# Performance work log

Hardware: AMD Instinct MI355X
Metric: run time of the kernel (lower is better)

Reference implementation:

```python
import jax, jax.numpy as jnp
import numpy as np

D_MODEL = 1024
D_FF = 4096
NUM_EXPERTS = 8
TOP_K = 2


def setup_inputs() -> dict:
    key = jax.random.key(0)
    ks = jax.random.split(key, 9)
    s_in = 1.0 / np.sqrt(D_MODEL)
    s_ff = 1.0 / np.sqrt(D_FF)
    return {
        "x": jax.random.normal(ks[0], (2, 1024, D_MODEL), dtype=jnp.float32),
        "Wg": jax.random.uniform(ks[1], (D_MODEL, NUM_EXPERTS), minval=-s_in, maxval=s_in, dtype=jnp.float32),
        "bg": jax.random.uniform(ks[2], (NUM_EXPERTS,), minval=-s_in, maxval=s_in, dtype=jnp.float32),
        "W1": jax.random.uniform(ks[3], (NUM_EXPERTS, D_MODEL, D_FF), minval=-s_in, maxval=s_in, dtype=jnp.float32),
        "b1": jax.random.uniform(ks[4], (NUM_EXPERTS, D_FF), minval=-s_in, maxval=s_in, dtype=jnp.float32),
        "W2": jax.random.uniform(ks[5], (NUM_EXPERTS, D_MODEL, D_FF), minval=-s_in, maxval=s_in, dtype=jnp.float32),
        "b2": jax.random.uniform(ks[6], (NUM_EXPERTS, D_FF), minval=-s_in, maxval=s_in, dtype=jnp.float32),
        "W3": jax.random.uniform(ks[7], (NUM_EXPERTS, D_FF, D_MODEL), minval=-s_ff, maxval=s_ff, dtype=jnp.float32),
        "b3": jax.random.uniform(ks[8], (NUM_EXPERTS, D_MODEL), minval=-s_ff, maxval=s_ff, dtype=jnp.float32),
    }


def reference(x, Wg, bg, W1, b1, W2, b2, W3, b3):
    B, S, D = x.shape
    xf = x.reshape(-1, D)                                   # [N, D]
    N = xf.shape[0]

    # ---- Router (eval mode: no noise) ----
    logits = xf @ Wg + bg                                   # [N, E]
    top_logits, top_idx = jax.lax.top_k(logits, TOP_K)      # [N, K]
    top_w = jax.nn.softmax(top_logits, axis=-1)             # softmax over the top-k logits
    # scatter top-k weights into dense [N, E]; indices are unique per row
    comb_w = jnp.zeros_like(logits).at[jnp.arange(N)[:, None], top_idx].set(top_w)

    # ---- Experts: GLU-MLP, dense per-expert (weights are 0 for unrouted tokens) ----
    h1 = jnp.einsum('nd,edf->enf', xf, W1) + b1[:, None, :]  # [E, N, F]
    h2 = jnp.einsum('nd,edf->enf', xf, W2) + b2[:, None, :]
    hidden = jax.nn.gelu(h1, approximate=False) * h2         # torch nn.GELU is exact (erf)
    expert_out = jnp.einsum('enf,efd->end', hidden, W3) + b3[:, None, :]  # [E, N, D]

    # ---- Weighted combine ----
    final = jnp.einsum('end,ne->nd', expert_out, comb_w)     # [N, D]
    aux_loss = 0.0  # eval mode: aux loss inactive
    return final.reshape(B, S, D), aux_loss
```

## Files before the change

### kernel.cpp

```cpp
#include <hip/hip_runtime.h>
#include <hip/hip_bf16.h>
#include <math.h>

#define D_MODEL 1024
#define D_FF    4096
#define NE      8
#define MT      256

typedef __bf16 bf16x8 __attribute__((ext_vector_type(8)));
typedef float  f32x4  __attribute__((ext_vector_type(4)));

__device__ __forceinline__ void async16(const void* g, void* l) {
    __builtin_amdgcn_global_load_lds(
        (__attribute__((address_space(1))) uint32_t*)g,
        (__attribute__((address_space(3))) uint32_t*)l, 16, 0, 0);
}

__device__ __forceinline__ void transpose_tile64(
    const float* __restrict__ s, __bf16* __restrict__ d,
    int K, int N, int kt, int nt, int tid, float (*tile)[65])
{
    int tr = tid >> 4, tc = (tid & 15) * 4;
#pragma unroll
    for (int it = 0; it < 4; ++it) {
        float4 v = *reinterpret_cast<const float4*>(
            s + (size_t)(kt + tr + it * 16) * N + nt + tc);
        tile[tr + it * 16][tc + 0] = v.x;
        tile[tr + it * 16][tc + 1] = v.y;
        tile[tr + it * 16][tc + 2] = v.z;
        tile[tr + it * 16][tc + 3] = v.w;
    }
    __syncthreads();
    int kq = (tid & 15) * 4;
#pragma unroll
    for (int it = 0; it < 4; ++it) {
        int rr = (tid >> 4) + it * 16;
        union { __bf16 h[4]; ushort4 u; } pk;
        pk.h[0] = (__bf16)tile[kq + 0][rr];
        pk.h[1] = (__bf16)tile[kq + 1][rr];
        pk.h[2] = (__bf16)tile[kq + 2][rr];
        pk.h[3] = (__bf16)tile[kq + 3][rr];
        *reinterpret_cast<ushort4*>(d + (size_t)(nt + rr) * K + kt + kq) = pk.u;
    }
}

__global__ __launch_bounds__(256) void fused_pre(
    const float* __restrict__ x, const float* __restrict__ Wg,
    const float* __restrict__ bg, int* __restrict__ topidx,
    float* __restrict__ topw, __bf16* __restrict__ Xb,
    const float* __restrict__ W1, const float* __restrict__ W2,
    const float* __restrict__ W3,
    __bf16* __restrict__ W1t, __bf16* __restrict__ W2t,
    __bf16* __restrict__ W3t, int nrouter)
{
    __shared__ float buf[64][65];
    int bid = blockIdx.x, tid = threadIdx.x;

    if (bid >= nrouter) {
        int tt = bid - nrouter;
        if (tt < 2 * 8192) {
            const float* s = W1; __bf16* d = W1t;
            if (tt >= 8192) { s = W2; d = W2t; tt -= 8192; }
            int e = tt >> 10, rem = tt & 1023;
            int kt_i = rem >> 6, nt_i = rem & 63;
            transpose_tile64(s + ((size_t)e << 22), d + ((size_t)e << 22),
                             D_MODEL, D_FF, kt_i * 64, nt_i * 64, tid, buf);
        } else {
            tt -= 2 * 8192;
            int e = tt >> 10, rem = tt & 1023;
            int kt_i = rem >> 4, nt_i = rem & 15;
            transpose_tile64(W3 + ((size_t)e << 22), W3t + ((size_t)e << 22),
                             D_FF, D_MODEL, kt_i * 64, nt_i * 64, tid, buf);
        }
        return;
    }

    int n = bid;
    const float* xr = x + (size_t)n * D_MODEL;
    int d0 = tid * 4;
    float4 xv = *reinterpret_cast<const float4*>(xr + d0);

    union { __bf16 h[4]; ushort4 u; } pk;
    pk.h[0] = (__bf16)xv.x; pk.h[1] = (__bf16)xv.y;
    pk.h[2] = (__bf16)xv.z; pk.h[3] = (__bf16)xv.w;
    *reinterpret_cast<ushort4*>(Xb + (size_t)n * D_MODEL + d0) = pk.u;

    float part[NE];
#pragma unroll
    for (int e = 0; e < NE; ++e) part[e] = 0.f;
    float xs[4] = {xv.x, xv.y, xv.z, xv.w};
#pragma unroll
    for (int j = 0; j < 4; ++j) {
        const float4* wr = reinterpret_cast<const float4*>(Wg + (size_t)(d0 + j) * NE);
        float4 w0 = wr[0], w1 = wr[1];
        part[0] += xs[j] * w0.x; part[1] += xs[j] * w0.y;
        part[2] += xs[j] * w0.z; part[3] += xs[j] * w0.w;
        part[4] += xs[j] * w1.x; part[5] += xs[j] * w1.y;
        part[6] += xs[j] * w1.z; part[7] += xs[j] * w1.w;
    }
#pragma unroll
    for (int off = 32; off > 0; off >>= 1) {
#pragma unroll
        for (int e = 0; e < NE; ++e) part[e] += __shfl_down(part[e], off);
    }
    float* sred = &buf[0][0];
    float* slog = &buf[1][0];
    int wave = tid >> 6, lane = tid & 63;
    if (lane == 0) {
#pragma unroll
        for (int e = 0; e < NE; ++e) sred[wave * NE + e] = part[e];
    }
    __syncthreads();
    if (tid < NE)
        slog[tid] = bg[tid] + sred[tid] + sred[NE + tid] + sred[2 * NE + tid] + sred[3 * NE + tid];
    __syncthreads();
    if (tid == 0) {
        float m0 = -1e30f, m1 = -1e30f; int i0 = 0, i1 = 0;
        for (int e = 0; e < NE; ++e) {
            float l = slog[e];
            if (l > m0)      { m1 = m0; i1 = i0; m0 = l; i0 = e; }
            else if (l > m1) { m1 = l;  i1 = e; }
        }
        float w1 = expf(m1 - m0);
        float s  = 1.f + w1;
        topidx[n * 2 + 0] = i0; topidx[n * 2 + 1] = i1;
        topw[n * 2 + 0] = 1.f / s; topw[n * 2 + 1] = w1 / s;
    }
}

__global__ __launch_bounds__(256) void build_lists_kernel(
    const int* __restrict__ topidx, const float* __restrict__ topw,
    int* __restrict__ pairTok, float* __restrict__ pairW,
    int* __restrict__ rbe, int* __restrict__ pairRow,
    int npairs, int maxrows, int maxblk)
{
    __shared__ int cnt[NE], cur[NE], pof[NE];
    int tid = threadIdx.x;
    if (tid < NE) { cnt[tid] = 0; cur[tid] = 0; }
    for (int i = tid; i < maxrows; i += 256) pairTok[i] = -1;
    for (int i = tid; i < maxblk; i += 256) rbe[i] = -1;
    __syncthreads();
    for (int p = tid; p < npairs; p += 256) atomicAdd(&cnt[topidx[p]], 1);
    __syncthreads();
    if (tid == 0) {
        int off = 0;
        for (int e = 0; e < NE; ++e) { pof[e] = off; off += (cnt[e] + MT - 1) & ~(MT - 1); }
        for (int e = 0; e < NE; ++e) {
            int nb = (cnt[e] + MT - 1) / MT;
            for (int j = 0; j < nb; ++j) rbe[pof[e] / MT + j] = e;
        }
    }
    __syncthreads();
    for (int p = tid; p < npairs; p += 256) {
        int e = topidx[p];
        int pos = atomicAdd(&cur[e], 1);
        int r = pof[e] + pos;
        pairTok[r]  = p >> 1;
        pairW[r]    = topw[p];
        pairRow[p]  = r;
    }
}

__global__ __launch_bounds__(512) void gemm1_mfma(
    const __bf16* __restrict__ Xb, const __bf16* __restrict__ W1t,
    const __bf16* __restrict__ W2t, const float* __restrict__ b1,
    const float* __restrict__ b2, const int* __restrict__ pairTok,
    const int* __restrict__ rbe, const __bf16* __restrict__ zpg,
    __bf16* __restrict__ hidden)
{
    int b = blockIdx.x;
    int e = rbe[b];
    if (e < 0) return;
    int fblk = blockIdx.y * 128;

    __shared__ __bf16 smem[2][32768];

    int tid = threadIdx.x, w = tid >> 6, l = tid & 63;
    int srcslot = (l & 7) ^ (l >> 3);
    int r0 = b * MT;

    const __bf16* aptr[4];
#pragma unroll
    for (int j = 0; j < 4; ++j) {
        int row = w * 32 + j * 8 + (l >> 3);
        int tok = pairTok[r0 + row];
        aptr[j] = (tok >= 0 ? Xb + (size_t)tok * D_MODEL : zpg) + srcslot * 8;
    }
    const __bf16* b1base = W1t + ((size_t)e << 22)
        + (size_t)(fblk + w * 16 + (l >> 3)) * D_MODEL + srcslot * 8;
    const __bf16* b2base = W2t + ((size_t)e << 22)
        + (size_t)(fblk + w * 16 + (l >> 3)) * D_MODEL + srcslot * 8;

    int wm = (w >> 1) * 64, wf = (w & 1) * 64;
    int lm = l & 15;

    f32x4 c1[4][4], c2[4][4];
#pragma unroll
    for (int mi = 0; mi < 4; ++mi)
#pragma unroll
        for (int fj = 0; fj < 4; ++fj) {
            c1[mi][fj] = (f32x4){0.f, 0.f, 0.f, 0.f};
            c2[mi][fj] = (f32x4){0.f, 0.f, 0.f, 0.f};
        }

    auto stage = [&](int buf, int k0) {
        __bf16* base = &smem[buf][0];
#pragma unroll
        for (int j = 0; j < 4; ++j)
            async16(aptr[j] + k0, base + w * 2048 + j * 512);
        async16(b1base + k0,               base + 16384 + w * 1024);
        async16(b1base + 8 * D_MODEL + k0, base + 16384 + w * 1024 + 512);
        async16(b2base + k0,               base + 24576 + w * 1024);
        async16(b2base + 8 * D_MODEL + k0, base + 24576 + w * 1024 + 512);
    };

    stage(0, 0);
    __syncthreads();
    const int NT = D_MODEL / 64;
    for (int t = 0; t < NT; ++t) {
        int cur = t & 1;
        if (t + 1 < NT) stage(cur ^ 1, (t + 1) * 64);
        const __bf16* sb = &smem[cur][0];
#pragma unroll
        for (int ks = 0; ks < 2; ++ks) {
            int sl = (((ks * 4 + (l >> 4)) ^ (l & 7)) << 3);
            bf16x8 a[4];
#pragma unroll
            for (int mi = 0; mi < 4; ++mi)
                a[mi] = *reinterpret_cast<const bf16x8*>(sb + (wm + mi * 16 + lm) * 64 + sl);
#pragma unroll
            for (int fj = 0; fj < 4; ++fj) {
                int frow = wf + fj * 16 + lm;
                bf16x8 bv1 = *reinterpret_cast<const bf16x8*>(sb + 16384 + frow * 64 + sl);
                bf16x8 bv2 = *reinterpret_cast<const bf16x8*>(sb + 24576 + frow * 64 + sl);
#pragma unroll
                for (int mi = 0; mi < 4; ++mi) {
                    c1[mi][fj] = __builtin_amdgcn_mfma_f32_16x16x32_bf16(a[mi], bv1, c1[mi][fj], 0, 0, 0);
                    c2[mi][fj] = __builtin_amdgcn_mfma_f32_16x16x32_bf16(a[mi], bv2, c2[mi][fj], 0, 0, 0);
                }
            }
        }
        __syncthreads();
    }

#pragma unroll
    for (int fj = 0; fj < 4; ++fj) {
        int f = fblk + wf + fj * 16 + lm;
        float b1v = b1[e * D_FF + f];
        float b2v = b2[e * D_FF + f];
#pragma unroll
        for (int mi = 0; mi < 4; ++mi)
#pragma unroll
            for (int r = 0; r < 4; ++r) {
                int m = wm + mi * 16 + (l >> 4) * 4 + r;
                float h1 = c1[mi][fj][r] + b1v;
                float h2 = c2[mi][fj][r] + b2v;
                float g = 0.5f * h1 * (1.f + erff(h1 * 0.70710678118654752f));
                hidden[(size_t)(r0 + m) * D_FF + f] = (__bf16)(g * h2);
            }
    }
}

__global__ __launch_bounds__(512, 4) void gemm2_mfma(
    const __bf16* __restrict__ hidden, const __bf16* __restrict__ W3t,
    const float* __restrict__ b3, const int* __restrict__ rbe,
    float* __restrict__ po)
{
    int rb = blockIdx.x;
    int e = rbe[rb >> 1];
    if (e < 0) return;
    int dblk = blockIdx.y * 128;

    __shared__ __bf16 smem[2][16384];

    int tid = threadIdx.x, w = tid >> 6, l = tid & 63;
    int ss8 = (l & 7) ^ (l >> 3);
    int r0m = rb * 128;

    const __bf16* abase = hidden + (size_t)(r0m + w * 16 + (l >> 3)) * D_FF + ss8 * 8;
    const __bf16* bbase = W3t + ((size_t)e << 22)
        + (size_t)(dblk + w * 16 + (l >> 3)) * D_FF + ss8 * 8;

    int wm = (w >> 1) * 32, wn = (w & 1) * 64;
    int lm = l & 15;

    f32x4 c[2][4];
#pragma unroll
    for (int mi = 0; mi < 2; ++mi)
#pragma unroll
        for (int nj = 0; nj < 4; ++nj) c[mi][nj] = (f32x4){0.f, 0.f, 0.f, 0.f};

    auto stage = [&](int buf, int k0) {
        __bf16* base = &smem[buf][0];
        async16(abase + k0,              base + w * 1024 + l * 8);
        async16(abase + 8 * D_FF + k0,   base + w * 1024 + 512 + l * 8);
        async16(bbase + k0,              base + 8192 + w * 1024 + l * 8);
        async16(bbase + 8 * D_FF + k0,   base + 8192 + w * 1024 + 512 + l * 8);
    };

    stage(0, 0);
    __syncthreads();
    const int NT = D_FF / 64;
    for (int t = 0; t < NT; ++t) {
        int cur = t & 1;
        if (t + 1 < NT) stage(cur ^ 1, (t + 1) * 64);
        const __bf16* sb = &smem[cur][0];
#pragma unroll
        for (int ks = 0; ks < 2; ++ks) {
            int sl = (((ks * 4 + (l >> 4)) ^ (l & 7)) << 3);
            bf16x8 a[2];
#pragma unroll
            for (int mi = 0; mi < 2; ++mi)
                a[mi] = *reinterpret_cast<const bf16x8*>(sb + (wm + mi * 16 + lm) * 64 + sl);
#pragma unroll
            for (int nj = 0; nj < 4; ++nj) {
                bf16x8 bv = *reinterpret_cast<const bf16x8*>(sb + 8192 + (wn + nj * 16 + lm) * 64 + sl);
#pragma unroll
                for (int mi = 0; mi < 2; ++mi)
                    c[mi][nj] = __builtin_amdgcn_mfma_f32_16x16x32_bf16(a[mi], bv, c[mi][nj], 0, 0, 0);
            }
        }
        __syncthreads();
    }

#pragma unroll
    for (int nj = 0; nj < 4; ++nj) {
        int d = dblk + wn + nj * 16 + lm;
        float b3v = b3[e * D_MODEL + d];
#pragma unroll
        for (int mi = 0; mi < 2; ++mi)
#pragma unroll
            for (int r = 0; r < 4; ++r) {
                int m = wm + mi * 16 + (l >> 4) * 4 + r;
                po[(size_t)(r0m + m) * D_MODEL + d] = c[mi][nj][r] + b3v;
            }
    }
}

__global__ __launch_bounds__(256) void combine_kernel(
    const float* __restrict__ po, const float* __restrict__ topw,
    const int* __restrict__ pairRow, float* __restrict__ out)
{
    int t = blockIdx.x, tid = threadIdx.x;
    int d = tid * 4;
    float w0 = topw[t * 2], w1 = topw[t * 2 + 1];
    int r0 = pairRow[t * 2], r1 = pairRow[t * 2 + 1];
    float4 v0 = *reinterpret_cast<const float4*>(po + (size_t)r0 * D_MODEL + d);
    float4 v1 = *reinterpret_cast<const float4*>(po + (size_t)r1 * D_MODEL + d);
    float4 o;
    o.x = w0 * v0.x + w1 * v1.x;
    o.y = w0 * v0.y + w1 * v1.y;
    o.z = w0 * v0.z + w1 * v1.z;
    o.w = w0 * v0.w + w1 * v1.w;
    *reinterpret_cast<float4*>(out + (size_t)t * D_MODEL + d) = o;
}

extern "C" void kernel_launch(void* const* d_in, const int* in_sizes, int n_in,
                              void* d_out, int out_size, void* d_ws, size_t ws_size,
                              hipStream_t stream)
{
    const float* x  = (const float*)d_in[0];
    const float* Wg = (const float*)d_in[1];
    const float* bg = (const float*)d_in[2];
    const float* W1 = (const float*)d_in[3];
    const float* b1 = (const float*)d_in[4];
    const float* W2 = (const float*)d_in[5];
    const float* b2 = (const float*)d_in[6];
    const float* W3 = (const float*)d_in[7];
    const float* b3 = (const float*)d_in[8];
    float* out = (float*)d_out;

    int N = in_sizes[0] / D_MODEL;
    int npairs = N * 2;
    int maxblk = npairs / MT + NE;
    int maxrows = maxblk * MT;

    char* ws = (char*)d_ws;
    size_t off = 0;
    auto alloc = [&](size_t bytes) -> void* {
        void* p = ws + off;
        off = (off + bytes + 255) & ~(size_t)255;
        return p;
    };
    int*    topidx  = (int*)   alloc((size_t)npairs * 4);
    float*  topw    = (float*) alloc((size_t)npairs * 4);
    int*    pairTok = (int*)   alloc((size_t)maxrows * 4);
    float*  pairW   = (float*) alloc((size_t)maxrows * 4);
    int*    rbe     = (int*)   alloc((size_t)maxblk * 4);
    int*    pairRow = (int*)   alloc((size_t)npairs * 4);
    __bf16* Xb      = (__bf16*)alloc((size_t)N * D_MODEL * 2);
    __bf16* hidden  = (__bf16*)alloc((size_t)maxrows * D_FF * 2);
    __bf16* zpg     = (__bf16*)alloc(4096);
    const size_t WSZ = (size_t)NE * D_MODEL * D_FF * 2;
    __bf16* W1t = (__bf16*)alloc(WSZ);
    __bf16* W2t = (__bf16*)alloc(WSZ);
    __bf16* W3t = (__bf16*)alloc(WSZ);
    float*  po  = (float*)W1t;
    (void)ws_size; (void)n_in; (void)pairW;

    hipMemsetAsync(zpg, 0, 4096, stream);

    fused_pre<<<N + 3 * 8192, 256, 0, stream>>>(
        x, Wg, bg, topidx, topw, Xb, W1, W2, W3, W1t, W2t, W3t, N);
    build_lists_kernel<<<1, 256, 0, stream>>>(topidx, topw, pairTok, pairW, rbe,
                                              pairRow, npairs, maxrows, maxblk);
    gemm1_mfma<<<dim3(maxblk, D_FF / 128), 512, 0, stream>>>(
        Xb, W1t, W2t, b1, b2, pairTok, rbe, zpg, hidden);
    gemm2_mfma<<<dim3(maxblk * 2, D_MODEL / 128), 512, 0, stream>>>(
        hidden, W3t, b3, rbe, po);
    combine_kernel<<<N, 256, 0, stream>>>(po, topw, pairRow, out);
}
```

Before: 335.0 us.

## Halve gemm1 K-tile to 32 to cut LDS and request higher occupancy

Shrinks the gemm1 LDS double buffer by staging 32-wide K slices instead of 64, with a new XOR swizzle and load mapping to suit. The launch-bounds hint now asks for up to 4 resident blocks per CU. The aim is to fit multiple blocks per CU so loads and compute can overlap across blocks. The trade-off is twice as many barrier iterations. The aggressive min-blocks hint may also force register spills, given the large accumulator state.

```diff
diff --git a/kernel.cpp b/kernel.cpp
--- a/kernel.cpp
+++ b/kernel.cpp
@@ -161,7 +161,7 @@
     }
 }
 
-__global__ __launch_bounds__(512) void gemm1_mfma(
+__global__ __launch_bounds__(512, 4) void gemm1_mfma(
     const __bf16* __restrict__ Xb, const __bf16* __restrict__ W1t,
     const __bf16* __restrict__ W2t, const float* __restrict__ b1,
     const float* __restrict__ b2, const int* __restrict__ pairTok,
@@ -173,26 +173,26 @@
     if (e < 0) return;
     int fblk = blockIdx.y * 128;
 
-    __shared__ __bf16 smem[2][32768];
+    __shared__ __bf16 smem[2][16384];
 
     int tid = threadIdx.x, w = tid >> 6, l = tid & 63;
-    int srcslot = (l & 7) ^ (l >> 3);
+    int srcslot = (l & 3) ^ ((l >> 3) & 3);
     int r0 = b * MT;
 
-    const __bf16* aptr[4];
-#pragma unroll
-    for (int j = 0; j < 4; ++j) {
-        int row = w * 32 + j * 8 + (l >> 3);
+    const __bf16* aptr[2];
+#pragma unroll
+    for (int j = 0; j < 2; ++j) {
+        int row = w * 32 + j * 16 + (l >> 2);
         int tok = pairTok[r0 + row];
         aptr[j] = (tok >= 0 ? Xb + (size_t)tok * D_MODEL : zpg) + srcslot * 8;
     }
-    const __bf16* b1base = W1t + ((size_t)e << 22)
-        + (size_t)(fblk + w * 16 + (l >> 3)) * D_MODEL + srcslot * 8;
-    const __bf16* b2base = W2t + ((size_t)e << 22)
-        + (size_t)(fblk + w * 16 + (l >> 3)) * D_MODEL + srcslot * 8;
+    int wrow = fblk + w * 16 + (l >> 2);
+    const __bf16* b1ptr = W1t + ((size_t)e << 22) + (size_t)wrow * D_MODEL + srcslot * 8;
+    const __bf16* b2ptr = W2t + ((size_t)e << 22) + (size_t)wrow * D_MODEL + srcslot * 8;
 
     int wm = (w >> 1) * 64, wf = (w & 1) * 64;
     int lm = l & 15;
+    int sl = (((l >> 4) ^ ((lm >> 1) & 3)) << 3);
 
     f32x4 c1[4][4], c2[4][4];
 #pragma unroll
@@ -205,39 +205,32 @@
 
     auto stage = [&](int buf, int k0) {
         __bf16* base = &smem[buf][0];
-#pragma unroll
-        for (int j = 0; j < 4; ++j)
-            async16(aptr[j] + k0, base + w * 2048 + j * 512);
-        async16(b1base + k0,               base + 16384 + w * 1024);
-        async16(b1base + 8 * D_MODEL + k0, base + 16384 + w * 1024 + 512);
-        async16(b2base + k0,               base + 24576 + w * 1024);
-        async16(b2base + 8 * D_MODEL + k0, base + 24576 + w * 1024 + 512);
+        async16(aptr[0] + k0, base + w * 1024 + l * 8);
+        async16(aptr[1] + k0, base + w * 1024 + 512 + l * 8);
+        async16(b1ptr + k0, base + 8192 + w * 512 + l * 8);
+        async16(b2ptr + k0, base + 12288 + w * 512 + l * 8);
     };
 
     stage(0, 0);
     __syncthreads();
-    const int NT = D_MODEL / 64;
+    const int NT = D_MODEL / 32;
     for (int t = 0; t < NT; ++t) {
         int cur = t & 1;
-        if (t + 1 < NT) stage(cur ^ 1, (t + 1) * 64);
+        if (t + 1 < NT) stage(cur ^ 1, (t + 1) * 32);
         const __bf16* sb = &smem[cur][0];
-#pragma unroll
-        for (int ks = 0; ks < 2; ++ks) {
-            int sl = (((ks * 4 + (l >> 4)) ^ (l & 7)) << 3);
-            bf16x8 a[4];
-#pragma unroll
-            for (int mi = 0; mi < 4; ++mi)
-                a[mi] = *reinterpret_cast<const bf16x8*>(sb + (wm + mi * 16 + lm) * 64 + sl);
-#pragma unroll
-            for (int fj = 0; fj < 4; ++fj) {
-                int frow = wf + fj * 16 + lm;
-                bf16x8 bv1 = *reinterpret_cast<const bf16x8*>(sb + 16384 + frow * 64 + sl);
-                bf16x8 bv2 = *reinterpret_cast<const bf16x8*>(sb + 24576 + frow * 64 + sl);
-#pragma unroll
-                for (int mi = 0; mi < 4; ++mi) {
-                    c1[mi][fj] = __builtin_amdgcn_mfma_f32_16x16x32_bf16(a[mi], bv1, c1[mi][fj], 0, 0, 0);
-                    c2[mi][fj] = __builtin_amdgcn_mfma_f32_16x16x32_bf16(a[mi], bv2, c2[mi][fj], 0, 0, 0);
-                }
+        bf16x8 a[4];
+#pragma unroll
+        for (int mi = 0; mi < 4; ++mi)
+            a[mi] = *reinterpret_cast<const bf16x8*>(sb + (wm + mi * 16 + lm) * 32 + sl);
+#pragma unroll
+        for (int fj = 0; fj < 4; ++fj) {
+            int frow = (wf + fj * 16 + lm) * 32 + sl;
+            bf16x8 bv1 = *reinterpret_cast<const bf16x8*>(sb + 8192 + frow);
+            bf16x8 bv2 = *reinterpret_cast<const bf16x8*>(sb + 12288 + frow);
+#pragma unroll
+            for (int mi = 0; mi < 4; ++mi) {
+                c1[mi][fj] = __builtin_amdgcn_mfma_f32_16x16x32_bf16(a[mi], bv1, c1[mi][fj], 0, 0, 0);
+                c2[mi][fj] = __builtin_amdgcn_mfma_f32_16x16x32_bf16(a[mi], bv2, c2[mi][fj], 0, 0, 0);
             }
         }
         __syncthreads();
```

Measured after the change: 970.5 us. +189.7%, slower.
